# Kernel optimization log

Measured on AMD Instinct MI355X. Metric: run time of the kernel, lower is better.

## Reference

```python
import jax, jax.numpy as jnp
import numpy as np

N = 50000      # nodes
F_IN = 500     # in_channels
MID = 64       # mid_layer_channel
H = 2          # heads
OUT = 40       # out_channels
E = 800000     # edges per order
ORDER = 3
NEG_SLOPE = 0.2


def _gat(x, edge_index, W, a_src, a_dst, b, concat):
    # PyG-style GATConv (eval mode, dropout off), with self loops.
    n = x.shape[0]
    heads, ch = a_src.shape
    h = (x @ W).reshape(n, heads, ch)                    # [N,H,C]
    loop = jnp.arange(n)
    src = jnp.concatenate([edge_index[0], loop])
    dst = jnp.concatenate([edge_index[1], loop])
    al_s = jnp.sum(h * a_src, axis=-1)                   # [N,H]
    al_d = jnp.sum(h * a_dst, axis=-1)                   # [N,H]
    e = jax.nn.leaky_relu(al_s[src] + al_d[dst], NEG_SLOPE)   # [Etot,H]
    m = jax.ops.segment_max(e, dst, num_segments=n)      # softmax over incoming edges per dst
    ex = jnp.exp(e - m[dst])
    den = jax.ops.segment_sum(ex, dst, num_segments=n)
    alpha = ex / (den[dst] + 1e-16)
    out = jax.ops.segment_sum(alpha[:, :, None] * h[src], dst, num_segments=n)  # [N,H,C]
    if concat:
        return out.reshape(n, heads * ch) + b
    return out.mean(axis=1) + b


def _aggr(states, Wmix, wfin):
    # NOrderAggrConv (depth=2): mix order states with [order,order] weights + ELU,
    # then reduce to a single state with a learned [order] combination.
    h = jnp.stack(states, axis=1)                        # [N,order,C]
    h = jax.nn.elu(jnp.einsum('nkc,kj->njc', h, Wmix))
    return jnp.einsum('nkc,k->nc', h, wfin)


def setup_inputs():
    key = jax.random.key(0)
    ks = jax.random.split(key, 40)
    d = {}
    d['node_feature'] = jax.random.normal(ks[0], (N, F_IN), jnp.float32)
    for o in range(ORDER):
        d[f'adj{o}'] = jax.random.randint(ks[1 + o], (2, E), 0, N)
    i = 4
    s = 0.05
    layer_dims = [(F_IN, MID, H * MID), (MID * H, OUT, OUT)]
    for l, (fin, c, bdim) in enumerate(layer_dims):
        for o in range(ORDER):
            d[f'W_{l}_{o}'] = jax.random.normal(ks[i], (fin, H * c), jnp.float32) * s; i += 1
            d[f'as_{l}_{o}'] = jax.random.normal(ks[i], (H, c), jnp.float32) * s; i += 1
            d[f'ad_{l}_{o}'] = jax.random.normal(ks[i], (H, c), jnp.float32) * s; i += 1
            d[f'b_{l}_{o}'] = jnp.zeros((bdim,), jnp.float32)
    for l in range(2):
        d[f'agg{l}_W'] = jax.random.normal(ks[i], (ORDER, ORDER), jnp.float32) * 0.5; i += 1
        d[f'agg{l}_w'] = jnp.full((ORDER,), 1.0 / ORDER, jnp.float32)
    return d


def reference(node_feature, adj0, adj1, adj2,
              W_0_0, as_0_0, ad_0_0, b_0_0,
              W_0_1, as_0_1, ad_0_1, b_0_1,
              W_0_2, as_0_2, ad_0_2, b_0_2,
              W_1_0, as_1_0, ad_1_0, b_1_0,
              W_1_1, as_1_1, ad_1_1, b_1_1,
              W_1_2, as_1_2, ad_1_2, b_1_2,
              agg0_W, agg0_w, agg1_W, agg1_w):
    adjs = (adj0, adj1, adj2)
    p0 = ((W_0_0, as_0_0, ad_0_0, b_0_0),
          (W_0_1, as_0_1, ad_0_1, b_0_1),
          (W_0_2, as_0_2, ad_0_2, b_0_2))
    p1 = ((W_1_0, as_1_0, ad_1_0, b_1_0),
          (W_1_1, as_1_1, ad_1_1, b_1_1),
          (W_1_2, as_1_2, ad_1_2, b_1_2))
    aggs = ((agg0_W, agg0_w), (agg1_W, agg1_w))
    x = node_feature  # eval mode: dropout is identity
    for l, params in enumerate((p0, p1)):
        concat = (l == 0)
        states = [jax.nn.elu(_gat(x, adjs[o], *params[o], concat)) for o in range(ORDER)]
        x = _aggr(states, *aggs[l])
    return jax.nn.log_softmax(x, axis=1)
```

## Files before the change

### kernel.cpp

```cpp
#include <hip/hip_runtime.h>
#include <cstdint>
#include <cstddef>
#include <math.h>


typedef __attribute__((ext_vector_type(8))) short short8;
typedef __attribute__((ext_vector_type(4))) float f32x4;
typedef __attribute__((ext_vector_type(2))) float f32x2;

struct P3f { const float* p[3]; };
struct P3c { const int* p[3]; };

__device__ __forceinline__ float leakyf(float x) { return x > 0.f ? x : 0.2f * x; }
__device__ __forceinline__ float eluf(float x)   { return x > 0.f ? x : expm1f(x); }

__device__ __forceinline__ unsigned short bf16r(float x) {
  unsigned int u = __float_as_uint(x);
  u += 0x7fffu + ((u >> 16) & 1u);
  return (unsigned short)(u >> 16);
}
__device__ __forceinline__ float bflo(unsigned int u) { return __uint_as_float(u << 16); }
__device__ __forceinline__ float bfhi(unsigned int u) { return __uint_as_float(u & 0xffff0000u); }

__device__ __forceinline__ void bf8_fma2(uint4 q, float xx, f32x2* a) {
  f32x2 v0 = {bflo(q.x), bfhi(q.x)};
  f32x2 v1 = {bflo(q.y), bfhi(q.y)};
  f32x2 v2 = {bflo(q.z), bfhi(q.z)};
  f32x2 v3 = {bflo(q.w), bfhi(q.w)};
  a[0] += xx * v0;
  a[1] += xx * v1;
  a[2] += xx * v2;
  a[3] += xx * v3;
}

__global__ __launch_bounds__(256) void zero_int_kernel(int* p, int n) {
  int i = blockIdx.x * blockDim.x + threadIdx.x;
  if (i < n) p[i] = 0;
}

__global__ __launch_bounds__(256) void count3_kernel(P3c adj, int* __restrict__ cntb,
                                                     int E, int N) {
  int i = blockIdx.x * blockDim.x + threadIdx.x;
  int o = blockIdx.y;
  if (i < E) atomicAdd(&cntb[o * N + adj.p[o][E + i]], 1);
}

#define SCAN_T 256
#define SCAN_VPT 8
#define SCAN_TILE 2048

__global__ __launch_bounds__(SCAN_T) void scan1_kernel(const int* __restrict__ cntb,
    int* __restrict__ rowptrb, int* __restrict__ bsums, int N) {
  __shared__ int lds[SCAN_T];
  const int o = blockIdx.y;
  const int* cnt = cntb + o * N;
  int* rowptr = rowptrb + o * (N + 1);
  int t = threadIdx.x;
  int base = blockIdx.x * SCAN_TILE + t * SCAN_VPT;
  int v[SCAN_VPT];
  int s = 0;
#pragma unroll
  for (int i = 0; i < SCAN_VPT; ++i) {
    int idx = base + i;
    int x = (idx < N) ? cnt[idx] : 0;
    s += x;
    v[i] = s;
  }
  lds[t] = s;
  __syncthreads();
  for (int off = 1; off < SCAN_T; off <<= 1) {
    int add = (t >= off) ? lds[t - off] : 0;
    __syncthreads();
    lds[t] += add;
    __syncthreads();
  }
  int excl = (t > 0) ? lds[t - 1] : 0;
#pragma unroll
  for (int i = 0; i < SCAN_VPT; ++i) {
    int idx = base + i;
    if (idx < N) rowptr[idx + 1] = excl + v[i];
  }
  if (t == SCAN_T - 1) bsums[o * 64 + blockIdx.x] = lds[t];
}

__global__ void scan2_kernel(int* bsums, int nb, int* rowptrb, int N) {
  if (threadIdx.x == 0 && blockIdx.x == 0) {
    for (int o = 0; o < 3; ++o) {
      int run = 0;
      for (int i = 0; i < nb; ++i) {
        int x = bsums[o * 64 + i];
        bsums[o * 64 + i] = run;
        run += x;
      }
      rowptrb[o * (N + 1)] = 0;
    }
  }
}

__global__ __launch_bounds__(256) void scan3_kernel(int* __restrict__ rowptrb,
    const int* __restrict__ bsums, int N) {
  int idx = blockIdx.x * blockDim.x + threadIdx.x;
  int o = blockIdx.y;
  if (idx < N) rowptrb[o * (N + 1) + idx + 1] += bsums[o * 64 + idx / SCAN_TILE];
}

__global__ __launch_bounds__(256) void fill3_kernel(P3c adj,
    const int* __restrict__ rowptrb, int* __restrict__ curb,
    int* __restrict__ colvb, int E, int N) {
  int i = blockIdx.x * blockDim.x + threadIdx.x;
  int o = blockIdx.y;
  if (i < E) {
    const int* a = adj.p[o];
    int d = a[E + i];
    int pos = atomicAdd(&curb[o * N + d], 1);
    colvb[(size_t)o * E + rowptrb[o * (N + 1) + d] + pos] = a[i];
  }
}

__global__ __launch_bounds__(256) void conv_bt3_kernel(P3f W,
    unsigned short* __restrict__ BtB, int K, int NC, int Kpad) {
  int n = blockIdx.y;
  int o = blockIdx.z;
  int k = blockIdx.x * 256 + threadIdx.x;
  if (k >= Kpad) return;
  float v = (k < K) ? W.p[o][(size_t)k * NC + n] : 0.f;
  BtB[(size_t)o * NC * Kpad + (size_t)n * Kpad + k] = bf16r(v);
}

#define GBM 128
#define LDSTRIDE 40

template<int NT>
__global__ __launch_bounds__(256) void mfma_gemm_kernel(
    const float* __restrict__ A, const unsigned short* __restrict__ BtB,
    P3f asp, P3f adp, unsigned short* __restrict__ CbB,
    float2* __restrict__ alsB, float2* __restrict__ aldB, int M, int K) {
  constexpr int NC = NT * 16;
  constexpr int CH = NT * 8;
  __shared__ unsigned short As[GBM * LDSTRIDE];
  __shared__ unsigned short Bs[NC * LDSTRIDE];
  const int t = threadIdx.x;
  const int o = blockIdx.y;
  const int wave = t >> 6, lane = t & 63;
  const int quad = lane >> 4, l16 = lane & 15;
  const int m0 = blockIdx.x * GBM;
  const int Kpad = (K + 31) & ~31;
  const unsigned short* Bt = BtB + (size_t)o * NC * Kpad;
  unsigned short* Cb = CbB + (size_t)o * M * NC;
  float2* al_s = alsB + (size_t)o * M;
  float2* al_d = aldB + (size_t)o * M;
  const float* a_src = asp.p[o];
  const float* a_dst = adp.p[o];

  f32x4 acc[2][NT];
#pragma unroll
  for (int i = 0; i < 2; ++i)
#pragma unroll
    for (int j = 0; j < NT; ++j) acc[i][j] = (f32x4){0.f, 0.f, 0.f, 0.f};

  const int arow = t >> 1;
  const int akoff = (t & 1) * 16;
  const int gm = m0 + arow;
  const float* arowp = A + (size_t)gm * K;
  const unsigned short* browp = Bt + (size_t)arow * Kpad;

  for (int k0 = 0; k0 < Kpad; k0 += 32) {
    if (k0) __syncthreads();
    {
      float v[16];
      const int kb = k0 + akoff;
      if (gm < M && kb + 16 <= K) {
        const float4* p = (const float4*)(arowp + kb);
#pragma unroll
        for (int i = 0; i < 4; ++i) {
          float4 q = p[i];
          v[4 * i] = q.x; v[4 * i + 1] = q.y; v[4 * i + 2] = q.z; v[4 * i + 3] = q.w;
        }
      } else {
#pragma unroll
        for (int i = 0; i < 16; ++i)
          v[i] = (gm < M && kb + i < K) ? arowp[kb + i] : 0.f;
      }
      union { unsigned short u[16]; short8 s[2]; } pk;
#pragma unroll
      for (int i = 0; i < 16; ++i) pk.u[i] = bf16r(v[i]);
      short8* dst = (short8*)&As[arow * LDSTRIDE + akoff];
      dst[0] = pk.s[0];
      dst[1] = pk.s[1];
    }
    if (arow < NC) {
      const uint4* p = (const uint4*)(browp + k0 + akoff);
      uint4 q0 = p[0], q1 = p[1];
      short8* dst = (short8*)&Bs[arow * LDSTRIDE + akoff];
      union { uint4 q; short8 s; } c0, c1;
      c0.q = q0; c1.q = q1;
      dst[0] = c0.s;
      dst[1] = c1.s;
    }
    __syncthreads();
    short8 af[2];
#pragma unroll
    for (int rt = 0; rt < 2; ++rt)
      af[rt] = *(const short8*)&As[(wave * 32 + rt * 16 + l16) * LDSTRIDE + quad * 8];
    short8 bfv[NT];
#pragma unroll
    for (int ct = 0; ct < NT; ++ct)
      bfv[ct] = *(const short8*)&Bs[(ct * 16 + l16) * LDSTRIDE + quad * 8];
#pragma unroll
    for (int rt = 0; rt < 2; ++rt)
#pragma unroll
      for (int ct = 0; ct < NT; ++ct)
        acc[rt][ct] = __builtin_amdgcn_mfma_f32_16x16x32_bf16(af[rt], bfv[ct],
                                                              acc[rt][ct], 0, 0, 0);
  }
  float asv[NT], adv[NT];
#pragma unroll
  for (int ct = 0; ct < NT; ++ct) {
    int col = ct * 16 + l16;
    asv[ct] = a_src[col];
    adv[ct] = a_dst[col];
  }
#pragma unroll
  for (int rt = 0; rt < 2; ++rt) {
    int gr0 = m0 + wave * 32 + rt * 16 + quad * 4;
#pragma unroll
    for (int r = 0; r < 4; ++r) {
      int gr = gr0 + r;
      float ps0 = 0.f, ps1 = 0.f, pd0 = 0.f, pd1 = 0.f;
#pragma unroll
      for (int ct = 0; ct < NT; ++ct) {
        int col = ct * 16 + l16;
        float v = acc[rt][ct][r];
        if (gr < M) Cb[(size_t)gr * NC + col] = bf16r(v);
        if (col < CH) { ps0 += v * asv[ct]; pd0 += v * adv[ct]; }
        else          { ps1 += v * asv[ct]; pd1 += v * adv[ct]; }
      }
#pragma unroll
      for (int off = 1; off < 16; off <<= 1) {
        ps0 += __shfl_xor(ps0, off, 64);
        ps1 += __shfl_xor(ps1, off, 64);
        pd0 += __shfl_xor(pd0, off, 64);
        pd1 += __shfl_xor(pd1, off, 64);
      }
      if (l16 == 0 && gr < M) {
        al_s[gr] = make_float2(ps0, ps1);
        al_d[gr] = make_float2(pd0, pd1);
      }
    }
  }
}

template<int C, int CONCAT>
__global__ __launch_bounds__(256) void gat_aggr4_kernel(
    const unsigned short* __restrict__ hB, const float2* __restrict__ alsB,
    const float2* __restrict__ aldB, const int* __restrict__ rowptrB,
    const int* __restrict__ colvB, P3f biasp, unsigned short* __restrict__ outB,
    int N, int E) {
  constexpr int HC = 2 * C;
  constexpr int FL = HC / 8;
  constexpr int ES = 64 / FL;
  constexpr int HB = C / 8;
  constexpr int OW = CONCAT ? HC : C;
  const int o = blockIdx.y;
  const unsigned short* h = hB + (size_t)o * N * HC;
  const float2* al_s = alsB + (size_t)o * N;
  const float2* al_d = aldB + (size_t)o * N;
  const int* rowptr = rowptrB + o * (N + 1);
  const int* colv = colvB + (size_t)o * E;
  const float* bias = biasp.p[o];
  unsigned short* out = outB + (size_t)o * N * OW;

  int w = (blockIdx.x * blockDim.x + threadIdx.x) >> 6;
  int lane = threadIdx.x & 63;
  if (w >= N) return;
  const int eslot = lane / FL;
  const int f4 = lane - eslot * FL;
  const bool glane = lane < ES * FL;
  const float2 ad = al_d[w];
  const float2 asf = al_s[w];
  const int beg = rowptr[w], end = rowptr[w + 1];
  const int deg = end - beg;

  const float xs0 = __expf(leakyf(asf.x + ad.x));
  const float xs1 = __expf(leakyf(asf.y + ad.y));

  f32x2 acc[4] = {}, acc2[4] = {};
  float dp0 = 0.f, dp1 = 0.f;

  auto gstep = [&](int s_reg, float x0_reg, float x1_reg, int j, int cnt, f32x2* a) {
    int sj = __shfl(s_reg, j, 64);
    float xa = __shfl(x0_reg, j, 64);
    float xb = __shfl(x1_reg, j, 64);
    if (glane && j < cnt) {
      uint4 q = ((const uint4*)(h + (size_t)sj * HC))[f4];
      bf8_fma2(q, (f4 < HB) ? xa : xb, a);
    }
  };

  if (deg <= 64) {
    int i = beg + lane;
    bool in = i < end;
    int s = in ? colv[i] : 0;
    float2 a = in ? al_s[s] : make_float2(0.f, 0.f);
    float x0 = in ? __expf(leakyf(a.x + ad.x)) : 0.f;
    float x1 = in ? __expf(leakyf(a.y + ad.y)) : 0.f;
    dp0 = x0; dp1 = x1;
    for (int jj = 0; jj < deg; jj += 2 * ES) {
      gstep(s, x0, x1, jj + eslot, deg, acc);
      gstep(s, x0, x1, jj + ES + eslot, deg, acc2);
    }
  } else {
    for (int base = beg; base < end; base += 64) {
      int i = base + lane;
      bool in = i < end;
      int s = in ? colv[i] : 0;
      float2 a = in ? al_s[s] : make_float2(0.f, 0.f);
      float x0 = in ? __expf(leakyf(a.x + ad.x)) : 0.f;
      float x1 = in ? __expf(leakyf(a.y + ad.y)) : 0.f;
      dp0 += x0; dp1 += x1;
      int cnt = min(64, end - base);
      for (int jj = 0; jj < cnt; jj += 2 * ES) {
        gstep(s, x0, x1, jj + eslot, cnt, acc);
        gstep(s, x0, x1, jj + ES + eslot, cnt, acc2);
      }
    }
  }

#pragma unroll
  for (int off = 1; off < 64; off <<= 1) {
    dp0 += __shfl_xor(dp0, off, 64);
    dp1 += __shfl_xor(dp1, off, 64);
  }
  float den0 = dp0 + xs0, den1 = dp1 + xs1;

  if (eslot == 0) {
    uint4 q = ((const uint4*)(h + (size_t)w * HC))[f4];
    bf8_fma2(q, (f4 < HB) ? xs0 : xs1, acc);
  }
#pragma unroll
  for (int i = 0; i < 4; ++i) acc[i] += acc2[i];
#pragma unroll
  for (int k = 1; k < ES; ++k) {
#pragma unroll
    for (int i = 0; i < 4; ++i) {
      float t0 = __shfl(acc[i][0], lane + k * FL, 64);
      float t1 = __shfl(acc[i][1], lane + k * FL, 64);
      if (lane < FL) { acc[i][0] += t0; acc[i][1] += t1; }
    }
  }

  float inv0 = 1.f / (den0 + 1e-16f), inv1 = 1.f / (den1 + 1e-16f);
  if (CONCAT) {
    if (lane < FL) {
      float xx = (f4 < HB) ? inv0 : inv1;
      const float* bp = bias + f4 * 8;
      unsigned int pk[4];
#pragma unroll
      for (int i = 0; i < 4; ++i) {
        unsigned short lo = bf16r(eluf(acc[i][0] * xx + bp[2 * i]));
        unsigned short hi = bf16r(eluf(acc[i][1] * xx + bp[2 * i + 1]));
        pk[i] = (unsigned int)lo | ((unsigned int)hi << 16);
      }
      ((uint4*)(out + (size_t)w * OW + f4 * 8))[0] = make_uint4(pk[0], pk[1], pk[2], pk[3]);
    }
  } else {
    float p[8];
#pragma unroll
    for (int i = 0; i < 4; ++i) {
      p[2 * i]     = __shfl(acc[i][0], lane + HB, 64);
      p[2 * i + 1] = __shfl(acc[i][1], lane + HB, 64);
    }
    if (lane < HB) {
      const float* bp = bias + f4 * 8;
      unsigned int pk[4];
#pragma unroll
      for (int i = 0; i < 4; ++i) {
        float v0 = 0.5f * (acc[i][0] * inv0 + p[2 * i] * inv1) + bp[2 * i];
        float v1 = 0.5f * (acc[i][1] * inv0 + p[2 * i + 1] * inv1) + bp[2 * i + 1];
        pk[i] = (unsigned int)bf16r(eluf(v0)) | ((unsigned int)bf16r(eluf(v1)) << 16);
      }
      ((uint4*)(out + (size_t)w * OW + f4 * 8))[0] = make_uint4(pk[0], pk[1], pk[2], pk[3]);
    }
  }
}

__global__ __launch_bounds__(256) void mixb_kernel(const unsigned short* __restrict__ sb,
    const float* __restrict__ Wm, const float* __restrict__ wf,
    float* __restrict__ out, int perU) {
  int i = blockIdx.x * blockDim.x + threadIdx.x;
  if (i >= perU) return;
  const unsigned int* sp = (const unsigned int*)sb;
  unsigned int u0 = sp[i];
  unsigned int u1 = sp[perU + i];
  unsigned int u2 = sp[2 * perU + i];
  float a0 = bflo(u0), a1 = bfhi(u0);
  float b0 = bflo(u1), b1 = bfhi(u1);
  float c0 = bflo(u2), c1 = bfhi(u2);
  float r0 = 0.f, r1 = 0.f;
#pragma unroll
  for (int j = 0; j < 3; ++j) {
    float w0 = Wm[j], w1 = Wm[3 + j], w2 = Wm[6 + j], wj = wf[j];
    r0 += wj * eluf(a0 * w0 + b0 * w1 + c0 * w2);
    r1 += wj * eluf(a1 * w0 + b1 * w1 + c1 * w2);
  }
  ((float2*)out)[i] = make_float2(r0, r1);
}

__global__ __launch_bounds__(256) void log_softmax_kernel(const float* __restrict__ x,
    float* __restrict__ out, int N, int C) {
  int w = (blockIdx.x * blockDim.x + threadIdx.x) >> 6;
  int lane = threadIdx.x & 63;
  if (w >= N) return;
  float v = (lane < C) ? x[(size_t)w * C + lane] : -INFINITY;
  float mx = v;
#pragma unroll
  for (int off = 1; off < 64; off <<= 1) mx = fmaxf(mx, __shfl_xor(mx, off, 64));
  float ex = (lane < C) ? expf(v - mx) : 0.f;
  float s = ex;
#pragma unroll
  for (int off = 1; off < 64; off <<= 1) s += __shfl_xor(s, off, 64);
  if (lane < C) out[(size_t)w * C + lane] = v - mx - logf(s);
}

extern "C" void kernel_launch(void* const* d_in, const int* in_sizes, int n_in,
                              void* d_out, int out_size, void* d_ws, size_t ws_size,
                              hipStream_t stream) {
  const int F_IN = 500;
  const int N = in_sizes[0] / F_IN;
  const int E = in_sizes[1] / 2;
  const int HC0 = 128;
  const int HC1 = 80;
  const int C1 = 40;
  const int K0pad = 512, K1pad = 128;

  const float* x0 = (const float*)d_in[0];
  P3c adj;
  adj.p[0] = (const int*)d_in[1];
  adj.p[1] = (const int*)d_in[2];
  adj.p[2] = (const int*)d_in[3];
  P3f W0p, as0p, ad0p, b0p, W1p, as1p, ad1p, b1p;
  for (int o = 0; o < 3; ++o) {
    W0p.p[o]  = (const float*)d_in[4 + 4 * o + 0];
    as0p.p[o] = (const float*)d_in[4 + 4 * o + 1];
    ad0p.p[o] = (const float*)d_in[4 + 4 * o + 2];
    b0p.p[o]  = (const float*)d_in[4 + 4 * o + 3];
    W1p.p[o]  = (const float*)d_in[16 + 4 * o + 0];
    as1p.p[o] = (const float*)d_in[16 + 4 * o + 1];
    ad1p.p[o] = (const float*)d_in[16 + 4 * o + 2];
    b1p.p[o]  = (const float*)d_in[16 + 4 * o + 3];
  }
  const float* agg0W = (const float*)d_in[28];
  const float* agg0w = (const float*)d_in[29];
  const float* agg1W = (const float*)d_in[30];
  const float* agg1w = (const float*)d_in[31];

  char* ws = (char*)d_ws;
  size_t off = 0;
  auto alloc = [&](size_t bytes) -> void* {
    off = (off + 255) & ~(size_t)255;
    void* p = ws + off;
    off += bytes;
    return p;
  };
  int* rowptrb = (int*)alloc((size_t)3 * (N + 1) * 4);
  int* colvb   = (int*)alloc((size_t)3 * E * 4);
  int* cntcur  = (int*)alloc((size_t)6 * N * 4);
  int* bsums   = (int*)alloc(3 * 64 * 4);
  unsigned short* hB  = (unsigned short*)alloc((size_t)3 * N * HC0 * 2);
  unsigned short* stB = (unsigned short*)alloc((size_t)3 * N * HC0 * 2);
  float* x1 = (float*)alloc((size_t)N * HC0 * 4);
  float* x2 = (float*)alloc((size_t)N * C1 * 4);
  float2* alsB = (float2*)alloc((size_t)3 * N * 8);
  float2* aldB = (float2*)alloc((size_t)3 * N * 8);
  unsigned short* Bt0B = (unsigned short*)alloc((size_t)3 * HC0 * K0pad * 2);
  unsigned short* Bt1B = (unsigned short*)alloc((size_t)3 * HC1 * K1pad * 2);
  (void)ws_size;

  const int TB = 256;
  const int nbE = (E + TB - 1) / TB;
  const int nbN = (N + TB - 1) / TB;
  const int scanBlocks = (N + SCAN_TILE - 1) / SCAN_TILE;
  const int waveBlocks = (int)(((size_t)N * 64 + TB - 1) / TB);
  const int gemmBlocks = (N + GBM - 1) / GBM;

  conv_bt3_kernel<<<dim3((K0pad + 255) / 256, HC0, 3), TB, 0, stream>>>(W0p, Bt0B, F_IN, HC0, K0pad);
  conv_bt3_kernel<<<dim3((K1pad + 255) / 256, HC1, 3), TB, 0, stream>>>(W1p, Bt1B, HC0, HC1, K1pad);

  zero_int_kernel<<<(6 * N + TB - 1) / TB, TB, 0, stream>>>(cntcur, 6 * N);
  count3_kernel<<<dim3(nbE, 3), TB, 0, stream>>>(adj, cntcur, E, N);
  scan1_kernel<<<dim3(scanBlocks, 3), SCAN_T, 0, stream>>>(cntcur, rowptrb, bsums, N);
  scan2_kernel<<<1, 64, 0, stream>>>(bsums, scanBlocks, rowptrb, N);
  scan3_kernel<<<dim3(nbN, 3), TB, 0, stream>>>(rowptrb, bsums, N);
  fill3_kernel<<<dim3(nbE, 3), TB, 0, stream>>>(adj, rowptrb, cntcur + 3 * N, colvb, E, N);

  mfma_gemm_kernel<8><<<dim3(gemmBlocks, 3), TB, 0, stream>>>(
      x0, Bt0B, as0p, ad0p, hB, alsB, aldB, N, F_IN);
  gat_aggr4_kernel<64, 1><<<dim3(waveBlocks, 3), TB, 0, stream>>>(
      hB, alsB, aldB, rowptrb, colvb, b0p, stB, N, E);
  mixb_kernel<<<((N * HC0 / 2) + TB - 1) / TB, TB, 0, stream>>>(
      stB, agg0W, agg0w, x1, N * HC0 / 2);

  mfma_gemm_kernel<5><<<dim3(gemmBlocks, 3), TB, 0, stream>>>(
      x1, Bt1B, as1p, ad1p, hB, alsB, aldB, N, HC0);
  gat_aggr4_kernel<40, 0><<<dim3(waveBlocks, 3), TB, 0, stream>>>(
      hB, alsB, aldB, rowptrb, colvb, b1p, stB, N, E);
  mixb_kernel<<<((N * C1 / 2) + TB - 1) / TB, TB, 0, stream>>>(
      stB, agg1W, agg1w, x2, N * C1 / 2);

  log_softmax_kernel<<<waveBlocks, TB, 0, stream>>>(x2, (float*)d_out, N, C1);
}
```

Baseline: 870.6 us.

## Precompute edge softmax weights, keep layer-1 input in bf16, tree-fold reductions

Fill now also records the destination row of each CSR edge. A new edge_w kernel precomputes exp(leaky(as+ad)) per edge into a float2 buffer, so the aggregation kernel reads per-edge source index and weight directly instead of shuffling them across lanes. The first-layer mix kernel now writes bf16 in place into the state buffer, and the second GEMM gets a bf16-A path that skips fp32 loads and conversion. The cross-slot partial-sum reduction becomes a tree fold. The trade-off is an extra edge pass that writes and reads about 19 MB per layer, plus a rowid array.

```diff
diff --git a/kernel.cpp b/kernel.cpp
--- a/kernel.cpp
+++ b/kernel.cpp
@@ -106,15 +106,31 @@
 
 __global__ __launch_bounds__(256) void fill3_kernel(P3c adj,
     const int* __restrict__ rowptrb, int* __restrict__ curb,
-    int* __restrict__ colvb, int E, int N) {
+    int* __restrict__ colvb, int* __restrict__ rowidb, int E, int N) {
   int i = blockIdx.x * blockDim.x + threadIdx.x;
   int o = blockIdx.y;
   if (i < E) {
     const int* a = adj.p[o];
     int d = a[E + i];
     int pos = atomicAdd(&curb[o * N + d], 1);
-    colvb[(size_t)o * E + rowptrb[o * (N + 1) + d] + pos] = a[i];
-  }
+    size_t base = (size_t)o * E + rowptrb[o * (N + 1) + d] + pos;
+    colvb[base] = a[i];
+    rowidb[base] = d;
+  }
+}
+
+__global__ __launch_bounds__(256) void edge_w_kernel(const int* __restrict__ colvb,
+    const int* __restrict__ rowidb, const float2* __restrict__ alsB,
+    const float2* __restrict__ aldB, float2* __restrict__ xeB, int E, int N) {
+  int i = blockIdx.x * blockDim.x + threadIdx.x;
+  int o = blockIdx.y;
+  if (i >= E) return;
+  size_t idx = (size_t)o * E + i;
+  int s = colvb[idx];
+  int d = rowidb[idx];
+  float2 a = alsB[(size_t)o * N + s];
+  float2 b = aldB[(size_t)o * N + d];
+  xeB[idx] = make_float2(__expf(leakyf(a.x + b.x)), __expf(leakyf(a.y + b.y)));
 }
 
 __global__ __launch_bounds__(256) void conv_bt3_kernel(P3f W,
@@ -130,9 +146,9 @@
 #define GBM 128
 #define LDSTRIDE 40
 
-template<int NT>
+template<int NT, bool ABF16>
 __global__ __launch_bounds__(256) void mfma_gemm_kernel(
-    const float* __restrict__ A, const unsigned short* __restrict__ BtB,
+    const void* __restrict__ Av, const unsigned short* __restrict__ BtB,
     P3f asp, P3f adp, unsigned short* __restrict__ CbB,
     float2* __restrict__ alsB, float2* __restrict__ aldB, int M, int K) {
   constexpr int NC = NT * 16;
@@ -161,14 +177,26 @@
   const int arow = t >> 1;
   const int akoff = (t & 1) * 16;
   const int gm = m0 + arow;
-  const float* arowp = A + (size_t)gm * K;
   const unsigned short* browp = Bt + (size_t)arow * Kpad;
 
   for (int k0 = 0; k0 < Kpad; k0 += 32) {
     if (k0) __syncthreads();
-    {
+    const int kb = k0 + akoff;
+    if constexpr (ABF16) {
+      const unsigned short* arowp = (const unsigned short*)Av + (size_t)gm * K;
+      uint4 q0 = {0, 0, 0, 0}, q1 = {0, 0, 0, 0};
+      if (gm < M) {
+        const uint4* p = (const uint4*)(arowp + kb);
+        q0 = p[0]; q1 = p[1];
+      }
+      short8* dst = (short8*)&As[arow * LDSTRIDE + akoff];
+      union { uint4 q; short8 s; } c0, c1;
+      c0.q = q0; c1.q = q1;
+      dst[0] = c0.s;
+      dst[1] = c1.s;
+    } else {
+      const float* arowp = (const float*)Av + (size_t)gm * K;
       float v[16];
-      const int kb = k0 + akoff;
       if (gm < M && kb + 16 <= K) {
         const float4* p = (const float4*)(arowp + kb);
 #pragma unroll
@@ -251,11 +279,11 @@
 }
 
 template<int C, int CONCAT>
-__global__ __launch_bounds__(256) void gat_aggr4_kernel(
+__global__ __launch_bounds__(256) void gat_aggr5_kernel(
     const unsigned short* __restrict__ hB, const float2* __restrict__ alsB,
     const float2* __restrict__ aldB, const int* __restrict__ rowptrB,
-    const int* __restrict__ colvB, P3f biasp, unsigned short* __restrict__ outB,
-    int N, int E) {
+    const int* __restrict__ colvB, const float2* __restrict__ xeB,
+    P3f biasp, unsigned short* __restrict__ outB, int N, int E) {
   constexpr int HC = 2 * C;
   constexpr int FL = HC / 8;
   constexpr int ES = 64 / FL;
@@ -266,7 +294,6 @@
   const float2* al_s = alsB + (size_t)o * N;
   const float2* al_d = aldB + (size_t)o * N;
   const int* rowptr = rowptrB + o * (N + 1);
-  const int* colv = colvB + (size_t)o * E;
   const float* bias = biasp.p[o];
   unsigned short* out = outB + (size_t)o * N * OW;
 
@@ -280,6 +307,8 @@
   const float2 asf = al_s[w];
   const int beg = rowptr[w], end = rowptr[w + 1];
   const int deg = end - beg;
+  const int* cp = colvB + (size_t)o * E + beg;
+  const float2* xp = xeB + (size_t)o * E + beg;
 
   const float xs0 = __expf(leakyf(asf.x + ad.x));
   const float xs1 = __expf(leakyf(asf.y + ad.y));
@@ -287,43 +316,19 @@
   f32x2 acc[4] = {}, acc2[4] = {};
   float dp0 = 0.f, dp1 = 0.f;
 
-  auto gstep = [&](int s_reg, float x0_reg, float x1_reg, int j, int cnt, f32x2* a) {
-    int sj = __shfl(s_reg, j, 64);
-    float xa = __shfl(x0_reg, j, 64);
-    float xb = __shfl(x1_reg, j, 64);
-    if (glane && j < cnt) {
+  auto gstep = [&](int j, f32x2* a) {
+    if (glane && j < deg) {
+      int sj = cp[j];
+      float2 x = xp[j];
       uint4 q = ((const uint4*)(h + (size_t)sj * HC))[f4];
-      bf8_fma2(q, (f4 < HB) ? xa : xb, a);
+      if (f4 == 0) { dp0 += x.x; dp1 += x.y; }
+      bf8_fma2(q, (f4 < HB) ? x.x : x.y, a);
     }
   };
 
-  if (deg <= 64) {
-    int i = beg + lane;
-    bool in = i < end;
-    int s = in ? colv[i] : 0;
-    float2 a = in ? al_s[s] : make_float2(0.f, 0.f);
-    float x0 = in ? __expf(leakyf(a.x + ad.x)) : 0.f;
-    float x1 = in ? __expf(leakyf(a.y + ad.y)) : 0.f;
-    dp0 = x0; dp1 = x1;
-    for (int jj = 0; jj < deg; jj += 2 * ES) {
-      gstep(s, x0, x1, jj + eslot, deg, acc);
-      gstep(s, x0, x1, jj + ES + eslot, deg, acc2);
-    }
-  } else {
-    for (int base = beg; base < end; base += 64) {
-      int i = base + lane;
-      bool in = i < end;
-      int s = in ? colv[i] : 0;
-      float2 a = in ? al_s[s] : make_float2(0.f, 0.f);
-      float x0 = in ? __expf(leakyf(a.x + ad.x)) : 0.f;
-      float x1 = in ? __expf(leakyf(a.y + ad.y)) : 0.f;
-      dp0 += x0; dp1 += x1;
-      int cnt = min(64, end - base);
-      for (int jj = 0; jj < cnt; jj += 2 * ES) {
-        gstep(s, x0, x1, jj + eslot, cnt, acc);
-        gstep(s, x0, x1, jj + ES + eslot, cnt, acc2);
-      }
-    }
+  for (int jj = 0; jj < deg; jj += 2 * ES) {
+    gstep(jj + eslot, acc);
+    gstep(jj + ES + eslot, acc2);
   }
 
 #pragma unroll
@@ -339,14 +344,22 @@
   }
 #pragma unroll
   for (int i = 0; i < 4; ++i) acc[i] += acc2[i];
-#pragma unroll
-  for (int k = 1; k < ES; ++k) {
+
+  auto fold = [&](int off, int lim) {
 #pragma unroll
     for (int i = 0; i < 4; ++i) {
-      float t0 = __shfl(acc[i][0], lane + k * FL, 64);
-      float t1 = __shfl(acc[i][1], lane + k * FL, 64);
-      if (lane < FL) { acc[i][0] += t0; acc[i][1] += t1; }
-    }
+      float t0 = __shfl(acc[i][0], lane + off, 64);
+      float t1 = __shfl(acc[i][1], lane + off, 64);
+      if (lane < lim) { acc[i][0] += t0; acc[i][1] += t1; }
+    }
+  };
+  if (ES == 4) {
+    fold(2 * FL, 2 * FL);
+    fold(FL, FL);
+  } else {
+    fold(3 * FL, 3 * FL);
+    fold(FL, FL);
+    fold(2 * FL, FL);
   }
 
   float inv0 = 1.f / (den0 + 1e-16f), inv1 = 1.f / (den1 + 1e-16f);
@@ -384,9 +397,10 @@
   }
 }
 
+template<int BF16OUT>
 __global__ __launch_bounds__(256) void mixb_kernel(const unsigned short* __restrict__ sb,
     const float* __restrict__ Wm, const float* __restrict__ wf,
-    float* __restrict__ out, int perU) {
+    void* __restrict__ out, int perU) {
   int i = blockIdx.x * blockDim.x + threadIdx.x;
   if (i >= perU) return;
   const unsigned int* sp = (const unsigned int*)sb;
@@ -403,7 +417,11 @@
     r0 += wj * eluf(a0 * w0 + b0 * w1 + c0 * w2);
     r1 += wj * eluf(a1 * w0 + b1 * w1 + c1 * w2);
   }
-  ((float2*)out)[i] = make_float2(r0, r1);
+  if (BF16OUT) {
+    ((unsigned int*)out)[i] = (unsigned int)bf16r(r0) | ((unsigned int)bf16r(r1) << 16);
+  } else {
+    ((float2*)out)[i] = make_float2(r0, r1);
+  }
 }
 
 __global__ __launch_bounds__(256) void log_softmax_kernel(const float* __restrict__ x,
@@ -464,14 +482,15 @@
   };
   int* rowptrb = (int*)alloc((size_t)3 * (N + 1) * 4);
   int* colvb   = (int*)alloc((size_t)3 * E * 4);
+  int* rowidb  = (int*)alloc((size_t)3 * E * 4);
   int* cntcur  = (int*)alloc((size_t)6 * N * 4);
   int* bsums   = (int*)alloc(3 * 64 * 4);
   unsigned short* hB  = (unsigned short*)alloc((size_t)3 * N * HC0 * 2);
   unsigned short* stB = (unsigned short*)alloc((size_t)3 * N * HC0 * 2);
-  float* x1 = (float*)alloc((size_t)N * HC0 * 4);
   float* x2 = (float*)alloc((size_t)N * C1 * 4);
   float2* alsB = (float2*)alloc((size_t)3 * N * 8);
   float2* aldB = (float2*)alloc((size_t)3 * N * 8);
+  float2* xeB  = (float2*)alloc((size_t)3 * E * 8);
   unsigned short* Bt0B = (unsigned short*)alloc((size_t)3 * HC0 * K0pad * 2);
   unsigned short* Bt1B = (unsigned short*)alloc((size_t)3 * HC1 * K1pad * 2);
   (void)ws_size;
@@ -491,20 +510,22 @@
   scan1_kernel<<<dim3(scanBlocks, 3), SCAN_T, 0, stream>>>(cntcur, rowptrb, bsums, N);
   scan2_kernel<<<1, 64, 0, stream>>>(bsums, scanBlocks, rowptrb, N);
   scan3_kernel<<<dim3(nbN, 3), TB, 0, stream>>>(rowptrb, bsums, N);
-  fill3_kernel<<<dim3(nbE, 3), TB, 0, stream>>>(adj, rowptrb, cntcur + 3 * N, colvb, E, N);
-
-  mfma_gemm_kernel<8><<<dim3(gemmBlocks, 3), TB, 0, stream>>>(
+  fill3_kernel<<<dim3(nbE, 3), TB, 0, stream>>>(adj, rowptrb, cntcur + 3 * N, colvb, rowidb, E, N);
+
+  mfma_gemm_kernel<8, false><<<dim3(gemmBlocks, 3), TB, 0, stream>>>(
       x0, Bt0B, as0p, ad0p, hB, alsB, aldB, N, F_IN);
-  gat_aggr4_kernel<64, 1><<<dim3(waveBlocks, 3), TB, 0, stream>>>(
-      hB, alsB, aldB, rowptrb, colvb, b0p, stB, N, E);
-  mixb_kernel<<<((N * HC0 / 2) + TB - 1) / TB, TB, 0, stream>>>(
-      stB, agg0W, agg0w, x1, N * HC0 / 2);
-
-  mfma_gemm_kernel<5><<<dim3(gemmBlocks, 3), TB, 0, stream>>>(
-      x1, Bt1B, as1p, ad1p, hB, alsB, aldB, N, HC0);
-  gat_aggr4_kernel<40, 0><<<dim3(waveBlocks, 3), TB, 0, stream>>>(
-      hB, alsB, aldB, rowptrb, colvb, b1p, stB, N, E);
-  mixb_kernel<<<((N * C1 / 2) + TB - 1) / TB, TB, 0, stream>>>(
+  edge_w_kernel<<<dim3(nbE, 3), TB, 0, stream>>>(colvb, rowidb, alsB, aldB, xeB, E, N);
+  gat_aggr5_kernel<64, 1><<<dim3(waveBlocks, 3), TB, 0, stream>>>(
+      hB, alsB, aldB, rowptrb, colvb, xeB, b0p, stB, N, E);
+  mixb_kernel<1><<<((N * HC0 / 2) + TB - 1) / TB, TB, 0, stream>>>(
+      stB, agg0W, agg0w, stB, N * HC0 / 2);
+
+  mfma_gemm_kernel<5, true><<<dim3(gemmBlocks, 3), TB, 0, stream>>>(
+      stB, Bt1B, as1p, ad1p, hB, alsB, aldB, N, HC0);
+  edge_w_kernel<<<dim3(nbE, 3), TB, 0, stream>>>(colvb, rowidb, alsB, aldB, xeB, E, N);
+  gat_aggr5_kernel<40, 0><<<dim3(waveBlocks, 3), TB, 0, stream>>>(
+      hB, alsB, aldB, rowptrb, colvb, xeB, b1p, stB, N, E);
+  mixb_kernel<0><<<((N * C1 / 2) + TB - 1) / TB, TB, 0, stream>>>(
       stB, agg1W, agg1w, x2, N * C1 / 2);
 
   log_softmax_kernel<<<waveBlocks, TB, 0, stream>>>(x2, (float*)d_out, N, C1);
```

After: 922.3 us. 1.06x slower.

## Pre-convert GEMM inputs to bf16, emit bf16 mix output, unroll aggregation

Applied to the files above, without the earlier changes.

Adds a kernel that converts the fp32 node features to a padded bf16 buffer once, so each of the three per-order GEMM passes reads half the bytes and skips per-tile conversion. The layer-0 mix kernel now writes bf16 in place into the state buffer, which the layer-1 GEMM reads directly, removing the fp32 intermediate. The GAT aggregation gather loop is unrolled to four edge steps, and the cross-slot reduction becomes a tree of shuffles. The cost is an extra launch and a 50MB bf16 buffer, and the in-place mix write relies on each thread touching only its own index.

```diff
diff --git a/kernel.cpp b/kernel.cpp
--- a/kernel.cpp
+++ b/kernel.cpp
@@ -36,6 +36,27 @@
 __global__ __launch_bounds__(256) void zero_int_kernel(int* p, int n) {
   int i = blockIdx.x * blockDim.x + threadIdx.x;
   if (i < n) p[i] = 0;
+}
+
+__global__ __launch_bounds__(256) void convA_kernel(const float* __restrict__ A,
+    unsigned short* __restrict__ Ab, int M, int K, int Kpad) {
+  int i = blockIdx.x * blockDim.x + threadIdx.x;
+  int row = i >> 6;
+  int koff = (i & 63) * 8;
+  if (row >= M) return;
+  const float* ap = A + (size_t)row * K;
+  unsigned short v[8];
+  if (koff + 8 <= K) {
+    float4 q0 = ((const float4*)(ap + koff))[0];
+    float4 q1 = ((const float4*)(ap + koff))[1];
+    v[0] = bf16r(q0.x); v[1] = bf16r(q0.y); v[2] = bf16r(q0.z); v[3] = bf16r(q0.w);
+    v[4] = bf16r(q1.x); v[5] = bf16r(q1.y); v[6] = bf16r(q1.z); v[7] = bf16r(q1.w);
+  } else {
+#pragma unroll
+    for (int k = 0; k < 8; ++k)
+      v[k] = (koff + k < K) ? bf16r(ap[koff + k]) : (unsigned short)0;
+  }
+  *(uint4*)(Ab + (size_t)row * Kpad + koff) = *(const uint4*)v;
 }
 
 __global__ __launch_bounds__(256) void count3_kernel(P3c adj, int* __restrict__ cntb,
@@ -132,9 +153,9 @@
 
 template<int NT>
 __global__ __launch_bounds__(256) void mfma_gemm_kernel(
-    const float* __restrict__ A, const unsigned short* __restrict__ BtB,
+    const unsigned short* __restrict__ Ab, const unsigned short* __restrict__ BtB,
     P3f asp, P3f adp, unsigned short* __restrict__ CbB,
-    float2* __restrict__ alsB, float2* __restrict__ aldB, int M, int K) {
+    float2* __restrict__ alsB, float2* __restrict__ aldB, int M, int Kpad) {
   constexpr int NC = NT * 16;
   constexpr int CH = NT * 8;
   __shared__ unsigned short As[GBM * LDSTRIDE];
@@ -144,7 +165,6 @@
   const int wave = t >> 6, lane = t & 63;
   const int quad = lane >> 4, l16 = lane & 15;
   const int m0 = blockIdx.x * GBM;
-  const int Kpad = (K + 31) & ~31;
   const unsigned short* Bt = BtB + (size_t)o * NC * Kpad;
   unsigned short* Cb = CbB + (size_t)o * M * NC;
   float2* al_s = alsB + (size_t)o * M;
@@ -161,35 +181,26 @@
   const int arow = t >> 1;
   const int akoff = (t & 1) * 16;
   const int gm = m0 + arow;
-  const float* arowp = A + (size_t)gm * K;
+  const unsigned short* arowp = Ab + (size_t)gm * Kpad;
   const unsigned short* browp = Bt + (size_t)arow * Kpad;
 
   for (int k0 = 0; k0 < Kpad; k0 += 32) {
     if (k0) __syncthreads();
+    const int kb = k0 + akoff;
     {
-      float v[16];
-      const int kb = k0 + akoff;
-      if (gm < M && kb + 16 <= K) {
-        const float4* p = (const float4*)(arowp + kb);
-#pragma unroll
-        for (int i = 0; i < 4; ++i) {
-          float4 q = p[i];
-          v[4 * i] = q.x; v[4 * i + 1] = q.y; v[4 * i + 2] = q.z; v[4 * i + 3] = q.w;
-        }
-      } else {
-#pragma unroll
-        for (int i = 0; i < 16; ++i)
-          v[i] = (gm < M && kb + i < K) ? arowp[kb + i] : 0.f;
-      }
-      union { unsigned short u[16]; short8 s[2]; } pk;
-#pragma unroll
-      for (int i = 0; i < 16; ++i) pk.u[i] = bf16r(v[i]);
+      uint4 q0 = {0, 0, 0, 0}, q1 = {0, 0, 0, 0};
+      if (gm < M) {
+        const uint4* p = (const uint4*)(arowp + kb);
+        q0 = p[0]; q1 = p[1];
+      }
       short8* dst = (short8*)&As[arow * LDSTRIDE + akoff];
-      dst[0] = pk.s[0];
-      dst[1] = pk.s[1];
+      union { uint4 q; short8 s; } c0, c1;
+      c0.q = q0; c1.q = q1;
+      dst[0] = c0.s;
+      dst[1] = c1.s;
     }
     if (arow < NC) {
-      const uint4* p = (const uint4*)(browp + k0 + akoff);
+      const uint4* p = (const uint4*)(browp + kb);
       uint4 q0 = p[0], q1 = p[1];
       short8* dst = (short8*)&Bs[arow * LDSTRIDE + akoff];
       union { uint4 q; short8 s; } c0, c1;
@@ -266,7 +277,6 @@
   const float2* al_s = alsB + (size_t)o * N;
   const float2* al_d = aldB + (size_t)o * N;
   const int* rowptr = rowptrB + o * (N + 1);
-  const int* colv = colvB + (size_t)o * E;
   const float* bias = biasp.p[o];
   unsigned short* out = outB + (size_t)o * N * OW;
 
@@ -280,6 +290,7 @@
   const float2 asf = al_s[w];
   const int beg = rowptr[w], end = rowptr[w + 1];
   const int deg = end - beg;
+  const int* colv = colvB + (size_t)o * E;
 
   const float xs0 = __expf(leakyf(asf.x + ad.x));
   const float xs1 = __expf(leakyf(asf.y + ad.y));
@@ -305,9 +316,11 @@
     float x0 = in ? __expf(leakyf(a.x + ad.x)) : 0.f;
     float x1 = in ? __expf(leakyf(a.y + ad.y)) : 0.f;
     dp0 = x0; dp1 = x1;
-    for (int jj = 0; jj < deg; jj += 2 * ES) {
+    for (int jj = 0; jj < deg; jj += 4 * ES) {
       gstep(s, x0, x1, jj + eslot, deg, acc);
       gstep(s, x0, x1, jj + ES + eslot, deg, acc2);
+      gstep(s, x0, x1, jj + 2 * ES + eslot, deg, acc);
+      gstep(s, x0, x1, jj + 3 * ES + eslot, deg, acc2);
     }
   } else {
     for (int base = beg; base < end; base += 64) {
@@ -319,9 +332,11 @@
       float x1 = in ? __expf(leakyf(a.y + ad.y)) : 0.f;
       dp0 += x0; dp1 += x1;
       int cnt = min(64, end - base);
-      for (int jj = 0; jj < cnt; jj += 2 * ES) {
+      for (int jj = 0; jj < cnt; jj += 4 * ES) {
         gstep(s, x0, x1, jj + eslot, cnt, acc);
         gstep(s, x0, x1, jj + ES + eslot, cnt, acc2);
+        gstep(s, x0, x1, jj + 2 * ES + eslot, cnt, acc);
+        gstep(s, x0, x1, jj + 3 * ES + eslot, cnt, acc2);
       }
     }
   }
@@ -339,14 +354,22 @@
   }
 #pragma unroll
   for (int i = 0; i < 4; ++i) acc[i] += acc2[i];
-#pragma unroll
-  for (int k = 1; k < ES; ++k) {
+
+  auto fold = [&](int off, int lim) {
 #pragma unroll
     for (int i = 0; i < 4; ++i) {
-      float t0 = __shfl(acc[i][0], lane + k * FL, 64);
-      float t1 = __shfl(acc[i][1], lane + k * FL, 64);
-      if (lane < FL) { acc[i][0] += t0; acc[i][1] += t1; }
-    }
+      float t0 = __shfl(acc[i][0], lane + off, 64);
+      float t1 = __shfl(acc[i][1], lane + off, 64);
+      if (lane < lim) { acc[i][0] += t0; acc[i][1] += t1; }
+    }
+  };
+  if (ES == 4) {
+    fold(2 * FL, 2 * FL);
+    fold(FL, FL);
+  } else {
+    fold(3 * FL, 3 * FL);
+    fold(FL, FL);
+    fold(2 * FL, FL);
   }
 
   float inv0 = 1.f / (den0 + 1e-16f), inv1 = 1.f / (den1 + 1e-16f);
@@ -384,9 +407,10 @@
   }
 }
 
+template<int BF16OUT>
 __global__ __launch_bounds__(256) void mixb_kernel(const unsigned short* __restrict__ sb,
     const float* __restrict__ Wm, const float* __restrict__ wf,
-    float* __restrict__ out, int perU) {
+    void* __restrict__ out, int perU) {
   int i = blockIdx.x * blockDim.x + threadIdx.x;
   if (i >= perU) return;
   const unsigned int* sp = (const unsigned int*)sb;
@@ -403,7 +427,11 @@
     r0 += wj * eluf(a0 * w0 + b0 * w1 + c0 * w2);
     r1 += wj * eluf(a1 * w0 + b1 * w1 + c1 * w2);
   }
-  ((float2*)out)[i] = make_float2(r0, r1);
+  if (BF16OUT) {
+    ((unsigned int*)out)[i] = (unsigned int)bf16r(r0) | ((unsigned int)bf16r(r1) << 16);
+  } else {
+    ((float2*)out)[i] = make_float2(r0, r1);
+  }
 }
 
 __global__ __launch_bounds__(256) void log_softmax_kernel(const float* __restrict__ x,
@@ -466,9 +494,9 @@
   int* colvb   = (int*)alloc((size_t)3 * E * 4);
   int* cntcur  = (int*)alloc((size_t)6 * N * 4);
   int* bsums   = (int*)alloc(3 * 64 * 4);
+  unsigned short* x0b = (unsigned short*)alloc((size_t)N * K0pad * 2);
   unsigned short* hB  = (unsigned short*)alloc((size_t)3 * N * HC0 * 2);
   unsigned short* stB = (unsigned short*)alloc((size_t)3 * N * HC0 * 2);
-  float* x1 = (float*)alloc((size_t)N * HC0 * 4);
   float* x2 = (float*)alloc((size_t)N * C1 * 4);
   float2* alsB = (float2*)alloc((size_t)3 * N * 8);
   float2* aldB = (float2*)alloc((size_t)3 * N * 8);
@@ -483,6 +511,8 @@
   const int waveBlocks = (int)(((size_t)N * 64 + TB - 1) / TB);
   const int gemmBlocks = (N + GBM - 1) / GBM;
 
+  convA_kernel<<<(int)(((size_t)N * 64 + TB - 1) / TB), TB, 0, stream>>>(
+      x0, x0b, N, F_IN, K0pad);
   conv_bt3_kernel<<<dim3((K0pad + 255) / 256, HC0, 3), TB, 0, stream>>>(W0p, Bt0B, F_IN, HC0, K0pad);
   conv_bt3_kernel<<<dim3((K1pad + 255) / 256, HC1, 3), TB, 0, stream>>>(W1p, Bt1B, HC0, HC1, K1pad);
 
@@ -494,17 +524,17 @@
   fill3_kernel<<<dim3(nbE, 3), TB, 0, stream>>>(adj, rowptrb, cntcur + 3 * N, colvb, E, N);
 
   mfma_gemm_kernel<8><<<dim3(gemmBlocks, 3), TB, 0, stream>>>(
-      x0, Bt0B, as0p, ad0p, hB, alsB, aldB, N, F_IN);
+      x0b, Bt0B, as0p, ad0p, hB, alsB, aldB, N, K0pad);
   gat_aggr4_kernel<64, 1><<<dim3(waveBlocks, 3), TB, 0, stream>>>(
       hB, alsB, aldB, rowptrb, colvb, b0p, stB, N, E);
-  mixb_kernel<<<((N * HC0 / 2) + TB - 1) / TB, TB, 0, stream>>>(
-      stB, agg0W, agg0w, x1, N * HC0 / 2);
+  mixb_kernel<1><<<((N * HC0 / 2) + TB - 1) / TB, TB, 0, stream>>>(
+      stB, agg0W, agg0w, stB, N * HC0 / 2);
 
   mfma_gemm_kernel<5><<<dim3(gemmBlocks, 3), TB, 0, stream>>>(
-      x1, Bt1B, as1p, ad1p, hB, alsB, aldB, N, HC0);
+      stB, Bt1B, as1p, ad1p, hB, alsB, aldB, N, K1pad);
   gat_aggr4_kernel<40, 0><<<dim3(waveBlocks, 3), TB, 0, stream>>>(
       hB, alsB, aldB, rowptrb, colvb, b1p, stB, N, E);
-  mixb_kernel<<<((N * C1 / 2) + TB - 1) / TB, TB, 0, stream>>>(
+  mixb_kernel<0><<<((N * C1 / 2) + TB - 1) / TB, TB, 0, stream>>>(
       stB, agg1W, agg1w, x2, N * C1 / 2);
 
   log_softmax_kernel<<<waveBlocks, TB, 0, stream>>>(x2, (float*)d_out, N, C1);
```

Result: no change. 854.2 us (-1.9%).
